# Kernel optimization log

Hardware: AMD Instinct MI355X
Metric: run time of the kernel (lower is better)

## Reference

```python
import jax, jax.numpy as jnp
import numpy as np

LOW_A, LOW_B = 32 // 4, 32 // 4  # spatial_shape=(32,32) default -> keep 8x8 low freqs


def _dct_basis(K, N, dtype):
    # Unnormalized DCT-II basis (torch_dct norm=None): C[k,n] = 2*cos(pi*(2n+1)k/(2N))
    n = jnp.arange(N, dtype=jnp.float32)
    k = jnp.arange(K, dtype=jnp.float32)
    return (2.0 * jnp.cos(jnp.pi * (2.0 * n[None, :] + 1.0) * k[:, None] / (2.0 * N))).astype(dtype)


def setup_inputs() -> dict:
    key = jax.random.key(0)
    delta = jax.random.normal(key, (256, 3, 256, 256), dtype=jnp.float32)
    return {"delta": delta}


def reference(delta):
    B, C, H, W = delta.shape
    Ch = _dct_basis(LOW_A, H, delta.dtype)  # [a, H]
    Cw = _dct_basis(LOW_B, W, delta.dtype)  # [b, W]
    # Equivalent to dct_2d(delta)[:, :, :a, :b]: truncated DCT along H then W.
    low = jnp.einsum('ih,nchw,jw->ncij', Ch, delta, Cw)  # [B, C, a, b]
    return jnp.abs(low).mean()
```

## Files before the change

kernel.cpp:

```cpp
#include <hip/hip_runtime.h>


#define INV_COUNT (1.0f / 49152.0f)

__global__ __launch_bounds__(256, 3) void lowfreq_main(
    const float* __restrict__ delta, float* __restrict__ out)
{
    __shared__ float c_row[256][8];
    __shared__ float c_col[8][256];
    __shared__ float pacc[4][64];

    const int t = threadIdx.x;
    const int wave = t >> 6;
    const int lane = t & 63;

    {
        const float base = 3.14159265358979323846f * (2.0f * (float)t + 1.0f)
                           * (1.0f / 512.0f);
        #pragma unroll
        for (int k = 0; k < 8; ++k) {
            const float v = 2.0f * cosf(base * (float)k);
            c_row[t][k] = v;
            c_col[k][t] = v;
        }
    }
    __syncthreads();

    const float* img = delta + (size_t)blockIdx.x * 65536;
    const float* gp  = img + (wave << 6) * 256 + lane;

    float u[4][8];
    #pragma unroll
    for (int c = 0; c < 4; ++c)
        #pragma unroll
        for (int i = 0; i < 8; ++i) u[c][i] = 0.0f;

    #pragma unroll 4
    for (int r = 0; r < 64; ++r) {
        const int h = (wave << 6) + r;
        const float x0 = gp[r * 256 + 0];
        const float x1 = gp[r * 256 + 64];
        const float x2 = gp[r * 256 + 128];
        const float x3 = gp[r * 256 + 192];
        const float4 cA = *reinterpret_cast<const float4*>(&c_row[h][0]);
        const float4 cB = *reinterpret_cast<const float4*>(&c_row[h][4]);
        const float cc[8] = {cA.x, cA.y, cA.z, cA.w, cB.x, cB.y, cB.z, cB.w};
        #pragma unroll
        for (int i = 0; i < 8; ++i) {
            u[0][i] = fmaf(cc[i], x0, u[0][i]);
            u[1][i] = fmaf(cc[i], x1, u[1][i]);
            u[2][i] = fmaf(cc[i], x2, u[2][i]);
            u[3][i] = fmaf(cc[i], x3, u[3][i]);
        }
    }

    float cw[4][8];
    #pragma unroll
    for (int c = 0; c < 4; ++c)
        #pragma unroll
        for (int j = 0; j < 8; ++j)
            cw[c][j] = c_col[j][(c << 6) + lane];

    float v[64];
    #pragma unroll
    for (int i = 0; i < 8; ++i)
        #pragma unroll
        for (int j = 0; j < 8; ++j) {
            float s = u[0][i] * cw[0][j];
            s = fmaf(u[1][i], cw[1][j], s);
            s = fmaf(u[2][i], cw[2][j], s);
            s = fmaf(u[3][i], cw[3][j], s);
            v[(i << 3) + j] = s;
        }

    #pragma unroll
    for (int s = 0; s < 6; ++s) {
        const int m = 1 << s;
        const bool bit = (lane & m) != 0;
        #pragma unroll
        for (int k = 0; k < (64 >> (s + 1)); ++k) {
            const float a = v[2 * k];
            const float b = v[2 * k + 1];
            const float keep = bit ? b : a;
            const float send = bit ? a : b;
            const float recv = __shfl_xor(send, m, 64);
            v[k] = keep + recv;
        }
    }

    pacc[wave][lane] = v[0];
    __syncthreads();

    if (t < 64) {
        const float s4 = pacc[0][t] + pacc[1][t] + pacc[2][t] + pacc[3][t];
        float a = fabsf(s4);
        #pragma unroll
        for (int m = 1; m < 64; m <<= 1) a += __shfl_xor(a, m, 64);
        if (t == 0) atomicAdd(out, a * INV_COUNT);
    }
}

extern "C" void kernel_launch(void* const* d_in, const int* in_sizes, int n_in,
                              void* d_out, int out_size, void* d_ws, size_t ws_size,
                              hipStream_t stream)
{
    const float* delta = (const float*)d_in[0];
    float* out = (float*)d_out;
    hipMemsetAsync(out, 0, sizeof(float) * (size_t)out_size, stream);
    lowfreq_main<<<768, 256, 0, stream>>>(delta, out);
}
```

Baseline: 47.37 us.

## Split each image across two blocks and reduce partials in a second kernel

Each image is now processed by two blocks, each covering half the rows, so the grid doubles to 1536 blocks for better occupancy and load balance across CUs. Partial 8x8 coefficient sums are written to workspace, and a second reduce kernel combines the halves, takes absolute values and accumulates the mean with atomics. The memset is replaced by a zero store in block 0, and the DCT basis is now built with a Chebyshev recurrence instead of eight cosf calls. The trade-off is an extra kernel launch and a workspace round trip in exchange for more parallelism.

```diff
diff --git a/kernel.cpp b/kernel.cpp
--- a/kernel.cpp
+++ b/kernel.cpp
@@ -4,7 +4,8 @@
 #define INV_COUNT (1.0f / 49152.0f)
 
 __global__ __launch_bounds__(256, 3) void lowfreq_main(
-    const float* __restrict__ delta, float* __restrict__ out)
+    const float* __restrict__ delta, float* __restrict__ ws,
+    float* __restrict__ out)
 {
     __shared__ float c_row[256][8];
     __shared__ float c_col[8][256];
@@ -13,21 +14,30 @@
     const int t = threadIdx.x;
     const int wave = t >> 6;
     const int lane = t & 63;
+    const int bid = blockIdx.x;
+    const int img = bid >> 1;
+    const int half = bid & 1;
 
     {
-        const float base = 3.14159265358979323846f * (2.0f * (float)t + 1.0f)
-                           * (1.0f / 512.0f);
+        const float a = 3.14159265358979323846f * (2.0f * (float)t + 1.0f)
+                        * (1.0f / 512.0f);
+        const float ca = cosf(a);
+        float ckm1 = 1.0f;
+        float ck   = ca;
+        c_row[t][0] = 2.0f;  c_col[0][t] = 2.0f;
+        c_row[t][1] = 2.0f * ca;  c_col[1][t] = 2.0f * ca;
         #pragma unroll
-        for (int k = 0; k < 8; ++k) {
-            const float v = 2.0f * cosf(base * (float)k);
-            c_row[t][k] = v;
-            c_col[k][t] = v;
+        for (int k = 2; k < 8; ++k) {
+            const float cn = 2.0f * ca * ck - ckm1;
+            ckm1 = ck; ck = cn;
+            c_row[t][k] = 2.0f * cn;
+            c_col[k][t] = 2.0f * cn;
         }
     }
     __syncthreads();
 
-    const float* img = delta + (size_t)blockIdx.x * 65536;
-    const float* gp  = img + (wave << 6) * 256 + lane;
+    const int row0 = (half << 7) + (wave << 5);
+    const float* gp = delta + (size_t)img * 65536 + (size_t)row0 * 256 + lane;
 
     float u[4][8];
     #pragma unroll
@@ -36,8 +46,8 @@
         for (int i = 0; i < 8; ++i) u[c][i] = 0.0f;
 
     #pragma unroll 4
-    for (int r = 0; r < 64; ++r) {
-        const int h = (wave << 6) + r;
+    for (int r = 0; r < 32; ++r) {
+        const int h = row0 + r;
         const float x0 = gp[r * 256 + 0];
         const float x1 = gp[r * 256 + 64];
         const float x2 = gp[r * 256 + 128];
@@ -93,11 +103,31 @@
 
     if (t < 64) {
         const float s4 = pacc[0][t] + pacc[1][t] + pacc[2][t] + pacc[3][t];
-        float a = fabsf(s4);
-        #pragma unroll
-        for (int m = 1; m < 64; m <<= 1) a += __shfl_xor(a, m, 64);
-        if (t == 0) atomicAdd(out, a * INV_COUNT);
+        ws[(size_t)bid * 64 + t] = s4;
+        if (bid == 0 && t == 0) out[0] = 0.0f;
     }
+}
+
+__global__ __launch_bounds__(256) void lowfreq_reduce(
+    const float* __restrict__ ws, float* __restrict__ out)
+{
+    __shared__ float acc[4];
+    const int t = threadIdx.x;
+    const int wave = t >> 6;
+    const int lane = t & 63;
+    const int g = blockIdx.x * 256 + t;
+    const int img = g >> 6;
+    const int slot = g & 63;
+
+    const float s = ws[(size_t)(2 * img) * 64 + slot]
+                  + ws[(size_t)(2 * img + 1) * 64 + slot];
+    float a = fabsf(s);
+    #pragma unroll
+    for (int m = 1; m < 64; m <<= 1) a += __shfl_xor(a, m, 64);
+    if (lane == 0) acc[wave] = a;
+    __syncthreads();
+    if (t == 0)
+        atomicAdd(out, (acc[0] + acc[1] + acc[2] + acc[3]) * INV_COUNT);
 }
 
 extern "C" void kernel_launch(void* const* d_in, const int* in_sizes, int n_in,
@@ -106,6 +136,7 @@
 {
     const float* delta = (const float*)d_in[0];
     float* out = (float*)d_out;
-    hipMemsetAsync(out, 0, sizeof(float) * (size_t)out_size, stream);
-    lowfreq_main<<<768, 256, 0, stream>>>(delta, out);
+    float* ws = (float*)d_ws;
+    lowfreq_main<<<1536, 256, 0, stream>>>(delta, ws, out);
+    lowfreq_reduce<<<192, 256, 0, stream>>>(ws, out);
 }
```

Result: faster. 40.48 us (-14.5%).
